# Kernel optimization log

Measured on AMD Instinct MI355X. Metric: run time of the kernel, lower is better.

The kernel has to match this reference:

```python
import jax, jax.numpy as jnp
import numpy as np

ACTION_SCALE = 0.01
LOG_STD_MIN, LOG_STD_MAX = -20.0, 2.0


def setup_inputs() -> dict:
    key = jax.random.key(0)
    k1, k2, k3 = jax.random.split(key, 3)
    B, N, D = 8, 1024, 128
    kv = jax.random.normal(k1, (B, N, 4 * D), dtype=jnp.float32)
    positions = jax.random.normal(k2, (B, N, 3), dtype=jnp.float32)
    eps = jax.random.normal(k3, (B, N, 3), dtype=jnp.float32)  # standard-normal sample for rsample
    return {"kv": kv, "positions": positions, "eps": eps}


def reference(kv, positions, eps):
    # Split Atomwise output into mean/std key-value embeddings: each [B, N, D]
    k_mu, v_mu, k_sigma, v_sigma = jnp.split(kv, 4, axis=-1)

    # Low-rank attention-like pairwise scores: [B, N, N]
    rel_shifts_mean = jnp.einsum("bid,bjd->bij", k_mu, v_mu)
    rel_shifts_log_std = jnp.einsum("bid,bjd->bij", k_sigma, v_sigma)

    # All-pairs unit displacement vectors: [B, N, N, 3]
    P = positions[:, :, None, :] - positions[:, None, :, :]
    norm = jnp.linalg.norm(P, axis=-1) + 1e-8
    P = P / norm[..., None]

    # Weighted sum over the j axis (torch dim=-2): [B, N, 3]
    actions_mean = jnp.einsum("bijc,bij->bic", P, rel_shifts_mean)
    actions_log_std = jnp.clip(
        jnp.einsum("bijc,bij->bic", P, rel_shifts_log_std), LOG_STD_MIN, LOG_STD_MAX
    )
    actions_std = jnp.exp(actions_log_std)

    # TanhNormal rsample (training branch) with externally supplied noise eps
    pre_tanh = actions_mean + actions_std * eps
    actions = jnp.tanh(pre_tanh)

    # Normal log-prob minus tanh log-det-Jacobian
    normal_lp = (
        -0.5 * ((pre_tanh - actions_mean) / actions_std) ** 2
        - actions_log_std
        - 0.5 * jnp.log(2.0 * jnp.pi)
    )
    log_det = (
        2.0 * jnp.log(2.0)
        + jax.nn.log_sigmoid(2.0 * pre_tanh)
        + jax.nn.log_sigmoid(-2.0 * pre_tanh)
    )
    log_prob = jnp.sum(normal_lp - log_det, axis=(1, 2))[:, None]  # [B, 1]

    actions = actions * ACTION_SCALE
    # change-of-variables correction for the action_scale factor
    n_dims = pre_tanh.shape[1] * pre_tanh.shape[2]
    log_prob = log_prob - n_dims * jnp.log(ACTION_SCALE)
    return actions, log_prob
```

## Files before the change

### kernel.cpp

```cpp
#include <hip/hip_runtime.h>
#include <math.h>


#define NTOK 1024
#define LPCONST 14147.0828114f

typedef __bf16 bf16x8 __attribute__((ext_vector_type(8)));
typedef float f32x4 __attribute__((ext_vector_type(4)));
typedef unsigned short ushort8v __attribute__((ext_vector_type(8)));
#define MFMA(a, b, c) __builtin_amdgcn_mfma_f32_16x16x32_bf16(a, b, c, 0, 0, 0)

__device__ __forceinline__ unsigned short to_bf16(float x) {
    return (unsigned short)((__float_as_uint(x) + 0x8000u) >> 16);
}

__device__ __forceinline__ ushort8v pack8(float4 a, float4 b) {
    ushort8v u;
    u[0] = to_bf16(a.x); u[1] = to_bf16(a.y); u[2] = to_bf16(a.z); u[3] = to_bf16(a.w);
    u[4] = to_bf16(b.x); u[5] = to_bf16(b.y); u[6] = to_bf16(b.z); u[7] = to_bf16(b.w);
    return u;
}

__global__ __launch_bounds__(256) void prepass_kernel(
    const float* __restrict__ kv, unsigned short* __restrict__ frag,
    float* __restrict__ out)
{
    if (blockIdx.x == 0 && threadIdx.x < 8)
        out[8 * NTOK * 3 + threadIdx.x] = LPCONST;

    const int b = blockIdx.x & 7;
    const int g = (blockIdx.x >> 3) * 256 + threadIdx.x;
    const int lane = g & 63;
    const int kc   = (g >> 6) & 3;
    const int tile = (g >> 8) & 63;

    const int row = tile * 16 + (lane & 15);
    const int kof = kc * 32 + (lane >> 4) * 8;
    const float* gp = kv + ((size_t)b * NTOK + row) * 512 + 128 + kof;
    const float4 m0 = *(const float4*)gp;
    const float4 m1 = *(const float4*)(gp + 4);
    const float4 s0 = *(const float4*)(gp + 256);
    const float4 s1 = *(const float4*)(gp + 260);

    unsigned short* cp = frag + (size_t)(b * 64 + tile) * 4096 + kc * 1024 + lane * 8;
    *(ushort8v*)(cp + 0)   = pack8(m0, m1);
    *(ushort8v*)(cp + 512) = pack8(s0, s1);
}

__global__ __launch_bounds__(512) void actor_kernel(
    const float* __restrict__ kv, const unsigned short* __restrict__ fragV,
    const float* __restrict__ pos, float* __restrict__ partial)
{
    const int t = threadIdx.x;
    const int w = t >> 6;
    const int lane = t & 63;
    const int q = lane >> 4;
    const int r16 = lane & 15;
    const int b   = blockIdx.x & 7;
    const int jh  = (blockIdx.x >> 3) & 3;
    const int ibx = blockIdx.x >> 5;
    const int i0 = ibx * 32;

    const float* kvb  = kv + (size_t)b * NTOK * 512;
    const float* posb = pos + (size_t)b * NTOK * 3;

    __shared__ __align__(16) unsigned short sK[8192];
    __shared__ __align__(16) float spi[32 * 3];
    __shared__ __align__(16) float spj[256 * 3];
    float* wacc = (float*)sK;

    {
        const int ri = t >> 4;
        const int cg = t & 15;
        const float* gp = kvb + (size_t)(i0 + ri) * 512 + cg * 8;
        const float4 m0 = *(const float4*)(gp);
        const float4 m1 = *(const float4*)(gp + 4);
        const float4 s0 = *(const float4*)(gp + 256);
        const float4 s1 = *(const float4*)(gp + 260);
        unsigned short* dp = sK + (ri >> 4) * 4096 + (cg >> 2) * 1024
                           + ((cg & 3) * 16 + (ri & 15)) * 8;
        *(ushort8v*)(dp)       = pack8(m0, m1);
        *(ushort8v*)(dp + 512) = pack8(s0, s1);
    }
    if (t < 216) {
        if (t < 24)  *(float4*)&spi[t * 4] = *(const float4*)&posb[i0 * 3 + t * 4];
        else { const int v = t - 24;
               *(float4*)&spj[v * 4] = *(const float4*)&posb[jh * 768 + v * 4]; }
    }
    __syncthreads();

    float pix[2], piy[2], piz[2];
    #pragma unroll
    for (int tile = 0; tile < 2; ++tile) {
        pix[tile] = spi[(tile * 16 + r16) * 3 + 0];
        piy[tile] = spi[(tile * 16 + r16) * 3 + 1];
        piz[tile] = spi[(tile * 16 + r16) * 3 + 2];
    }

    float am[2][3] = {};
    float al[2][3] = {};

    const int jtile0 = jh * 16 + w * 2;
    const unsigned short* vbase =
        fragV + (size_t)(b * 64 + jtile0) * 4096 + lane * 8;
    const int klofs = lane * 8;

    #pragma unroll
    for (int jt = 0; jt < 2; ++jt) {
        const unsigned short* vp = vbase + jt * 4096;
        f32x4 accm[2], accs[2];
        #pragma unroll
        for (int tile = 0; tile < 2; ++tile) {
            accm[tile] = (f32x4){0.f, 0.f, 0.f, 0.f};
            accs[tile] = (f32x4){0.f, 0.f, 0.f, 0.f};
        }
        #pragma unroll
        for (int kc = 0; kc < 4; ++kc) {
            const bf16x8 Vm = *(const bf16x8*)(vp + kc * 1024);
            const bf16x8 Vs = *(const bf16x8*)(vp + kc * 1024 + 512);
            #pragma unroll
            for (int tile = 0; tile < 2; ++tile) {
                const bf16x8 Km = *(const bf16x8*)&sK[tile * 4096 + kc * 1024 + klofs];
                const bf16x8 Ks = *(const bf16x8*)&sK[tile * 4096 + kc * 1024 + 512 + klofs];
                accm[tile] = MFMA(Vm, Km, accm[tile]);
                accs[tile] = MFMA(Vs, Ks, accs[tile]);
            }
        }
        const int jl = (w * 2 + jt) * 16 + q * 4;
        #pragma unroll
        for (int reg = 0; reg < 4; ++reg) {
            const float* pj = &spj[(jl + reg) * 3];
            const float pjx = pj[0], pjy = pj[1], pjz = pj[2];
            #pragma unroll
            for (int tile = 0; tile < 2; ++tile) {
                const float dx = pix[tile] - pjx;
                const float dy = piy[tile] - pjy;
                const float dz = piz[tile] - pjz;
                const float d2 = dx * dx + dy * dy + dz * dz;
                const float inv = d2 > 0.f ? rsqrtf(d2) : 0.f;
                const float wm = accm[tile][reg] * inv;
                const float ws = accs[tile][reg] * inv;
                am[tile][0] = fmaf(dx, wm, am[tile][0]);
                am[tile][1] = fmaf(dy, wm, am[tile][1]);
                am[tile][2] = fmaf(dz, wm, am[tile][2]);
                al[tile][0] = fmaf(dx, ws, al[tile][0]);
                al[tile][1] = fmaf(dy, ws, al[tile][1]);
                al[tile][2] = fmaf(dz, ws, al[tile][2]);
            }
        }
    }

    #pragma unroll
    for (int tile = 0; tile < 2; ++tile)
        #pragma unroll
        for (int c = 0; c < 3; ++c) {
            float vm = am[tile][c], vl = al[tile][c];
            vm += __shfl_xor(vm, 16, 64); vm += __shfl_xor(vm, 32, 64);
            vl += __shfl_xor(vl, 16, 64); vl += __shfl_xor(vl, 32, 64);
            am[tile][c] = vm; al[tile][c] = vl;
        }

    __syncthreads();
    if (lane < 16) {
        #pragma unroll
        for (int tile = 0; tile < 2; ++tile) {
            float* p = wacc + (w * 32 + tile * 16 + r16) * 6;
            p[0] = am[tile][0]; p[1] = am[tile][1]; p[2] = am[tile][2];
            p[3] = al[tile][0]; p[4] = al[tile][1]; p[5] = al[tile][2];
        }
    }
    __syncthreads();
    if (t < 192) {
        float v = 0.f;
        #pragma unroll
        for (int ww = 0; ww < 8; ++ww) v += wacc[ww * 192 + t];
        const int row = t / 6, c = t - row * 6;
        partial[((size_t)((jh * 8 + b) * NTOK) + i0 + row) * 6 + c] = v;
    }
}

__global__ __launch_bounds__(64) void actor_tail_kernel(
    const float* __restrict__ partial, const float* __restrict__ eps,
    float* __restrict__ out)
{
    const int b = blockIdx.x >> 4;
    const int i = (blockIdx.x & 15) * 64 + threadIdx.x;
    const int gi = b * NTOK + i;

    float am[3] = {}, al[3] = {};
    #pragma unroll
    for (int jh = 0; jh < 4; ++jh) {
        const float* p = partial + (((size_t)jh * 8 + b) * NTOK + i) * 6;
        const float2 v0 = *(const float2*)(p);
        const float2 v1 = *(const float2*)(p + 2);
        const float2 v2 = *(const float2*)(p + 4);
        am[0] += v0.x; am[1] += v0.y; am[2] += v1.x;
        al[0] += v1.y; al[1] += v2.x; al[2] += v2.y;
    }

    float lp = 0.f;
    #pragma unroll
    for (int c = 0; c < 3; ++c) {
        const float als = fminf(fmaxf(al[c], -20.f), 2.f);
        const float sd = __expf(als);
        const float e = eps[gi * 3 + c];
        const float pre = fmaf(sd, e, am[c]);
        const float a2 = 2.f * fabsf(pre);
        const float E = __expf(-a2);
        const float th = (1.f - E) / (1.f + E);
        out[gi * 3 + c] = copysignf(th, pre) * 0.01f;
        lp += fmaf(-0.5f * e, e, -als) - 2.3052328944f + a2 + 2.f * __logf(1.f + E);
    }

    #pragma unroll
    for (int m = 1; m < 64; m <<= 1) lp += __shfl_xor(lp, m, 64);
    if (threadIdx.x == 0) atomicAdd(out + NTOK * 8 * 3 + b, lp);
}

extern "C" void kernel_launch(void* const* d_in, const int* in_sizes, int n_in,
                              void* d_out, int out_size, void* d_ws, size_t ws_size,
                              hipStream_t stream) {
    const float* kv = (const float*)d_in[0];
    const float* pos = (const float*)d_in[1];
    const float* eps = (const float*)d_in[2];
    float* out = (float*)d_out;
    unsigned short* fragV = (unsigned short*)d_ws;
    float* partial = (float*)((char*)d_ws + 4194304);

    prepass_kernel<<<dim3(512), 256, 0, stream>>>(kv, fragV, out);
    actor_kernel<<<dim3(1024), 512, 0, stream>>>(kv, fragV, pos, partial);
    actor_tail_kernel<<<dim3(128), 64, 0, stream>>>(partial, eps, out);
}
```

Before: 85.08 us.

## Fuse tail epilogue into actor kernel by covering full j range per block

```diff
diff --git a/kernel.cpp b/kernel.cpp
--- a/kernel.cpp
+++ b/kernel.cpp
@@ -49,7 +49,8 @@
 
 __global__ __launch_bounds__(512) void actor_kernel(
     const float* __restrict__ kv, const unsigned short* __restrict__ fragV,
-    const float* __restrict__ pos, float* __restrict__ partial)
+    const float* __restrict__ pos, const float* __restrict__ eps,
+    float* __restrict__ out)
 {
     const int t = threadIdx.x;
     const int w = t >> 6;
@@ -57,164 +58,121 @@
     const int q = lane >> 4;
     const int r16 = lane & 15;
     const int b   = blockIdx.x & 7;
-    const int jh  = (blockIdx.x >> 3) & 3;
-    const int ibx = blockIdx.x >> 5;
-    const int i0 = ibx * 32;
+    const int ibx = blockIdx.x >> 3;
+    const int i0 = ibx * 16;
 
     const float* kvb  = kv + (size_t)b * NTOK * 512;
     const float* posb = pos + (size_t)b * NTOK * 3;
 
-    __shared__ __align__(16) unsigned short sK[8192];
-    __shared__ __align__(16) float spi[32 * 3];
-    __shared__ __align__(16) float spj[256 * 3];
+    __shared__ __align__(16) unsigned short sK[4096];
+    __shared__ __align__(16) float spj[NTOK * 3];
+    __shared__ __align__(16) float spi[48];
     float* wacc = (float*)sK;
 
     {
-        const int ri = t >> 4;
-        const int cg = t & 15;
-        const float* gp = kvb + (size_t)(i0 + ri) * 512 + cg * 8;
-        const float4 m0 = *(const float4*)(gp);
-        const float4 m1 = *(const float4*)(gp + 4);
-        const float4 s0 = *(const float4*)(gp + 256);
-        const float4 s1 = *(const float4*)(gp + 260);
-        unsigned short* dp = sK + (ri >> 4) * 4096 + (cg >> 2) * 1024
-                           + ((cg & 3) * 16 + (ri & 15)) * 8;
-        *(ushort8v*)(dp)       = pack8(m0, m1);
-        *(ushort8v*)(dp + 512) = pack8(s0, s1);
+        const int ri  = t >> 5;
+        const int cg  = t & 31;
+        const int arr = cg >> 4;
+        const int c2  = cg & 15;
+        const float* gp = kvb + (size_t)(i0 + ri) * 512 + arr * 256 + c2 * 8;
+        const float4 a0 = *(const float4*)gp;
+        const float4 a1 = *(const float4*)(gp + 4);
+        unsigned short* dp = sK + (c2 >> 2) * 1024 + arr * 512
+                           + ((c2 & 3) * 16 + ri) * 8;
+        *(ushort8v*)dp = pack8(a0, a1);
     }
-    if (t < 216) {
-        if (t < 24)  *(float4*)&spi[t * 4] = *(const float4*)&posb[i0 * 3 + t * 4];
-        else { const int v = t - 24;
-               *(float4*)&spj[v * 4] = *(const float4*)&posb[jh * 768 + v * 4]; }
-    }
+    for (int u = t; u < 768; u += 512)
+        *(float4*)&spj[u * 4] = *(const float4*)&posb[u * 4];
+    if (t < 12) *(float4*)&spi[t * 4] = *(const float4*)&posb[i0 * 3 + t * 4];
     __syncthreads();
 
-    float pix[2], piy[2], piz[2];
-    #pragma unroll
-    for (int tile = 0; tile < 2; ++tile) {
-        pix[tile] = spi[(tile * 16 + r16) * 3 + 0];
-        piy[tile] = spi[(tile * 16 + r16) * 3 + 1];
-        piz[tile] = spi[(tile * 16 + r16) * 3 + 2];
-    }
+    const float pix = spi[r16 * 3 + 0];
+    const float piy = spi[r16 * 3 + 1];
+    const float piz = spi[r16 * 3 + 2];
 
-    float am[2][3] = {};
-    float al[2][3] = {};
+    float am[3] = {}, al[3] = {};
 
-    const int jtile0 = jh * 16 + w * 2;
     const unsigned short* vbase =
-        fragV + (size_t)(b * 64 + jtile0) * 4096 + lane * 8;
+        fragV + (size_t)(b * 64 + w * 8) * 4096 + lane * 8;
     const int klofs = lane * 8;
 
-    #pragma unroll
-    for (int jt = 0; jt < 2; ++jt) {
-        const unsigned short* vp = vbase + jt * 4096;
-        f32x4 accm[2], accs[2];
-        #pragma unroll
-        for (int tile = 0; tile < 2; ++tile) {
-            accm[tile] = (f32x4){0.f, 0.f, 0.f, 0.f};
-            accs[tile] = (f32x4){0.f, 0.f, 0.f, 0.f};
-        }
+    #pragma unroll 2
+    for (int jt = 0; jt < 8; ++jt) {
+        const unsigned short* vp = vbase + (size_t)jt * 4096;
+        f32x4 accm = (f32x4){0.f, 0.f, 0.f, 0.f};
+        f32x4 accs = (f32x4){0.f, 0.f, 0.f, 0.f};
         #pragma unroll
         for (int kc = 0; kc < 4; ++kc) {
             const bf16x8 Vm = *(const bf16x8*)(vp + kc * 1024);
             const bf16x8 Vs = *(const bf16x8*)(vp + kc * 1024 + 512);
-            #pragma unroll
-            for (int tile = 0; tile < 2; ++tile) {
-                const bf16x8 Km = *(const bf16x8*)&sK[tile * 4096 + kc * 1024 + klofs];
-                const bf16x8 Ks = *(const bf16x8*)&sK[tile * 4096 + kc * 1024 + 512 + klofs];
-                accm[tile] = MFMA(Vm, Km, accm[tile]);
-                accs[tile] = MFMA(Vs, Ks, accs[tile]);
-            }
+            const bf16x8 Km = *(const bf16x8*)&sK[kc * 1024 + klofs];
+            const bf16x8 Ks = *(const bf16x8*)&sK[kc * 1024 + 512 + klofs];
+            accm = MFMA(Vm, Km, accm);
+            accs = MFMA(Vs, Ks, accs);
         }
-        const int jl = (w * 2 + jt) * 16 + q * 4;
+        const int jbase = (w * 8 + jt) * 16 + q * 4;
         #pragma unroll
         for (int reg = 0; reg < 4; ++reg) {
-            const float* pj = &spj[(jl + reg) * 3];
+            const float* pj = &spj[(jbase + reg) * 3];
             const float pjx = pj[0], pjy = pj[1], pjz = pj[2];
-            #pragma unroll
-            for (int tile = 0; tile < 2; ++tile) {
-                const float dx = pix[tile] - pjx;
-                const float dy = piy[tile] - pjy;
-                const float dz = piz[tile] - pjz;
-                const float d2 = dx * dx + dy * dy + dz * dz;
-                const float inv = d2 > 0.f ? rsqrtf(d2) : 0.f;
-                const float wm = accm[tile][reg] * inv;
-                const float ws = accs[tile][reg] * inv;
-                am[tile][0] = fmaf(dx, wm, am[tile][0]);
-                am[tile][1] = fmaf(dy, wm, am[tile][1]);
-                am[tile][2] = fmaf(dz, wm, am[tile][2]);
-                al[tile][0] = fmaf(dx, ws, al[tile][0]);
-                al[tile][1] = fmaf(dy, ws, al[tile][1]);
-                al[tile][2] = fmaf(dz, ws, al[tile][2]);
-            }
+            const float dx = pix - pjx;
+            const float dy = piy - pjy;
+            const float dz = piz - pjz;
+            const float d2 = dx * dx + dy * dy + dz * dz;
+            const float inv = d2 > 0.f ? rsqrtf(d2) : 0.f;
+            const float wm = accm[reg] * inv;
+            const float ws = accs[reg] * inv;
+            am[0] = fmaf(dx, wm, am[0]);
+            am[1] = fmaf(dy, wm, am[1]);
+            am[2] = fmaf(dz, wm, am[2]);
+            al[0] = fmaf(dx, ws, al[0]);
+            al[1] = fmaf(dy, ws, al[1]);
+            al[2] = fmaf(dz, ws, al[2]);
         }
     }
 
     #pragma unroll
-    for (int tile = 0; tile < 2; ++tile)
-        #pragma unroll
-        for (int c = 0; c < 3; ++c) {
-            float vm = am[tile][c], vl = al[tile][c];
-            vm += __shfl_xor(vm, 16, 64); vm += __shfl_xor(vm, 32, 64);
-            vl += __shfl_xor(vl, 16, 64); vl += __shfl_xor(vl, 32, 64);
-            am[tile][c] = vm; al[tile][c] = vl;
-        }
+    for (int c = 0; c < 3; ++c) {
+        float vm = am[c], vl = al[c];
+        vm += __shfl_xor(vm, 16, 64); vm += __shfl_xor(vm, 32, 64);
+        vl += __shfl_xor(vl, 16, 64); vl += __shfl_xor(vl, 32, 64);
+        am[c] = vm; al[c] = vl;
+    }
 
     __syncthreads();
     if (lane < 16) {
-        #pragma unroll
-        for (int tile = 0; tile < 2; ++tile) {
-            float* p = wacc + (w * 32 + tile * 16 + r16) * 6;
-            p[0] = am[tile][0]; p[1] = am[tile][1]; p[2] = am[tile][2];
-            p[3] = al[tile][0]; p[4] = al[tile][1]; p[5] = al[tile][2];
-        }
+        float* p = wacc + (w * 16 + r16) * 6;
+        p[0] = am[0]; p[1] = am[1]; p[2] = am[2];
+        p[3] = al[0]; p[4] = al[1]; p[5] = al[2];
     }
     __syncthreads();
-    if (t < 192) {
-        float v = 0.f;
-        #pragma unroll
-        for (int ww = 0; ww < 8; ++ww) v += wacc[ww * 192 + t];
-        const int row = t / 6, c = t - row * 6;
-        partial[((size_t)((jh * 8 + b) * NTOK) + i0 + row) * 6 + c] = v;
-    }
-}
-
-__global__ __launch_bounds__(64) void actor_tail_kernel(
-    const float* __restrict__ partial, const float* __restrict__ eps,
-    float* __restrict__ out)
-{
-    const int b = blockIdx.x >> 4;
-    const int i = (blockIdx.x & 15) * 64 + threadIdx.x;
-    const int gi = b * NTOK + i;
-
-    float am[3] = {}, al[3] = {};
-    #pragma unroll
-    for (int jh = 0; jh < 4; ++jh) {
-        const float* p = partial + (((size_t)jh * 8 + b) * NTOK + i) * 6;
-        const float2 v0 = *(const float2*)(p);
-        const float2 v1 = *(const float2*)(p + 2);
-        const float2 v2 = *(const float2*)(p + 4);
-        am[0] += v0.x; am[1] += v0.y; am[2] += v1.x;
-        al[0] += v1.y; al[1] += v2.x; al[2] += v2.y;
-    }
 
     float lp = 0.f;
-    #pragma unroll
-    for (int c = 0; c < 3; ++c) {
-        const float als = fminf(fmaxf(al[c], -20.f), 2.f);
+    if (t < 48) {
+        const int row = t / 3, c = t - row * 3;
+        float sam = 0.f, sal = 0.f;
+        #pragma unroll
+        for (int ww = 0; ww < 8; ++ww) {
+            const float* p = wacc + ((ww * 16 + row) * 6);
+            sam += p[c];
+            sal += p[3 + c];
+        }
+        const int gi = b * NTOK + i0 + row;
+        const float als = fminf(fmaxf(sal, -20.f), 2.f);
         const float sd = __expf(als);
         const float e = eps[gi * 3 + c];
-        const float pre = fmaf(sd, e, am[c]);
+        const float pre = fmaf(sd, e, sam);
         const float a2 = 2.f * fabsf(pre);
         const float E = __expf(-a2);
         const float th = (1.f - E) / (1.f + E);
         out[gi * 3 + c] = copysignf(th, pre) * 0.01f;
-        lp += fmaf(-0.5f * e, e, -als) - 2.3052328944f + a2 + 2.f * __logf(1.f + E);
+        lp = fmaf(-0.5f * e, e, -als) - 2.3052328944f + a2 + 2.f * __logf(1.f + E);
     }
-
-    #pragma unroll
-    for (int m = 1; m < 64; m <<= 1) lp += __shfl_xor(lp, m, 64);
-    if (threadIdx.x == 0) atomicAdd(out + NTOK * 8 * 3 + b, lp);
+    if (t < 64) {
+        #pragma unroll
+        for (int m = 1; m < 64; m <<= 1) lp += __shfl_xor(lp, m, 64);
+        if (t == 0) atomicAdd(out + NTOK * 8 * 3 + b, lp);
+    }
 }
 
 extern "C" void kernel_launch(void* const* d_in, const int* in_sizes, int n_in,
@@ -225,9 +183,7 @@
     const float* eps = (const float*)d_in[2];
     float* out = (float*)d_out;
     unsigned short* fragV = (unsigned short*)d_ws;
-    float* partial = (float*)((char*)d_ws + 4194304);
 
     prepass_kernel<<<dim3(512), 256, 0, stream>>>(kv, fragV, out);
-    actor_kernel<<<dim3(1024), 512, 0, stream>>>(kv, fragV, pos, partial);
-    actor_tail_kernel<<<dim3(128), 64, 0, stream>>>(partial, eps, out);
+    actor_kernel<<<dim3(512), 512, 0, stream>>>(kv, fragV, pos, eps, out);
 }
```

Result: no change. 85.84 us (+0.9%).
